# Optimization experiments

Measured on AMD Instinct MI355X. Metric: run time of the kernel, lower is better.

Reference implementation:

```python
import jax, jax.numpy as jnp
import numpy as np

NS, NT, E, B = 100000, 50000, 3200000, 16
F_E, F_XS, F_XT, F_U = 10, 10, 5, 10
H1 = F_E + F_XT            # 15, node_mlp_1 width
H2 = F_XS + 1 + 4 * H1 + F_U  # 81, node_mlp_2 input width


def leaky(x):
    return jnp.where(x > 0, x, 0.1 * x)


def setup_inputs() -> dict:
    key = jax.random.key(0)
    ks = jax.random.split(key, 16)
    s = 0.1
    return {
        "x_s": jax.random.normal(ks[0], (NS, F_XS), jnp.float32),
        "x_t": jax.random.normal(ks[1], (NT, F_XT), jnp.float32),
        "edge_attr": jax.random.normal(ks[2], (E, F_E), jnp.float32),
        "u": jax.random.normal(ks[3], (B, F_U), jnp.float32),
        "W1": jax.random.normal(ks[4], (H1, H1), jnp.float32) * s,
        "b1": jnp.zeros((H1,), jnp.float32),
        "W2": jax.random.normal(ks[5], (H1, H1), jnp.float32) * s,
        "b2": jnp.zeros((H1,), jnp.float32),
        "W3": jax.random.normal(ks[6], (H2, F_XS), jnp.float32) * s,
        "b3": jnp.zeros((F_XS,), jnp.float32),
        "W4": jax.random.normal(ks[7], (F_XS, F_XS), jnp.float32) * s,
        "b4": jnp.zeros((F_XS,), jnp.float32),
        "src_idx": jax.random.randint(ks[8], (E,), 0, NS, jnp.int32),
        "tgt_idx": jax.random.randint(ks[9], (E,), 0, NT, jnp.int32),
        "batch_s": jnp.sort(jax.random.randint(ks[10], (NS,), 0, B, jnp.int32)),
    }


def reference(x_s, x_t, edge_attr, u, W1, b1, W2, b2, W3, b3, W4, b4,
              src_idx, tgt_idx, batch_s):
    Ns = x_s.shape[0]
    # edge MLP: gather target features, concat edge attrs -> [E, 15]
    out = jnp.concatenate([x_t[tgt_idx], edge_attr], axis=1)
    out = leaky(out @ W1 + b1) @ W2 + b2

    # per-source-node counts; torch_scatter 'mean' divides by max(count, 1)
    n = jax.ops.segment_sum(jnp.ones((out.shape[0],), out.dtype), src_idx,
                            num_segments=Ns)
    denom = jnp.maximum(n, 1.0)[:, None]

    a = jax.ops.segment_sum(out, src_idx, num_segments=Ns) / denom           # mean
    m2 = jax.ops.segment_sum(out ** 2, src_idx, num_segments=Ns) / denom     # mean sq
    b = jnp.sqrt(1e-6 + jax.nn.relu(m2 - a ** 2))                            # std
    diff = out - a[src_idx]
    c = jax.ops.segment_sum(diff ** 3, src_idx, num_segments=Ns) / denom / b ** 3
    d = jax.ops.segment_sum(diff ** 4, src_idx, num_segments=Ns) / denom / b ** 4

    feat = jnp.concatenate([x_s, n[:, None], a, b, c, d, u[batch_s]], axis=1)  # [Ns, 81]
    return leaky(feat @ W3 + b3) @ W4 + b4
```

## Files before the change

### kernel.cpp

```cpp
#include <hip/hip_runtime.h>
#include <hip/hip_fp16.h>

#define H1 15
#define H2 81
#define FXS 10
#define FXT 5
#define FE 10
#define FU 10

#define BSH 7
#define NPB 128
#define MAXBUK 1024
#define ABLK 2048
#define TB1 1024
#define TBF 512
#define CAPS 5120

typedef _Float16 half4 __attribute__((ext_vector_type(4)));
typedef float floatx4 __attribute__((ext_vector_type(4)));
typedef unsigned int uint;
typedef unsigned short ushort;

__device__ __forceinline__ int sw(int row, int q) {
    return row * 8 + 2 * (q ^ ((row >> 2) & 3));
}

__global__ __launch_bounds__(256) void k_bhist(const int* __restrict__ src,
                                               int* __restrict__ bcnt, int E, int nbuk) {
    __shared__ int h[MAXBUK];
    for (int i = threadIdx.x; i < MAXBUK; i += 256) h[i] = 0;
    __syncthreads();
    for (int i = blockIdx.x * blockDim.x + threadIdx.x; i < E; i += gridDim.x * blockDim.x)
        atomicAdd(&h[src[i] >> BSH], 1);
    __syncthreads();
    for (int i = threadIdx.x; i < nbuk; i += 256)
        if (h[i]) atomicAdd(&bcnt[i], h[i]);
}

__global__ __launch_bounds__(1024) void k_bscan(const int* __restrict__ bcnt,
                                                int* __restrict__ boffs,
                                                int* __restrict__ bcur, int nbuk) {
    __shared__ int sc[MAXBUK];
    int t = threadIdx.x;
    int v = (t < nbuk) ? bcnt[t] : 0;
    sc[t] = v;
    __syncthreads();
    for (int d = 1; d < MAXBUK; d <<= 1) {
        int add = (t >= d) ? sc[t - d] : 0;
        __syncthreads();
        sc[t] += add;
        __syncthreads();
    }
    if (t < nbuk) { int o = sc[t] - v; boffs[t] = o; bcur[t] = o; }
}

__global__ __launch_bounds__(TB1, 8) void k_mlpbin(
    const float* __restrict__ x_t, const float* __restrict__ ea,
    const float* __restrict__ W1, const float* __restrict__ b1,
    const float* __restrict__ W2, const float* __restrict__ b2,
    const int* __restrict__ src, const int* __restrict__ tgt,
    int* __restrict__ bcur, uint* __restrict__ gbin, int E)
{
    __shared__ uint stagw[ABLK * 8];
    __shared__ int A[MAXBUK];
    __shared__ int B[MAXBUK];
    __shared__ ushort sbk[ABLK];
    __shared__ int wsum[16];

    int t = threadIdx.x;
    int lane = t & 63, w = t >> 6;
    int base = blockIdx.x * ABLK;
    int m = min(ABLK, E - base);

    int i0 = t, i1 = t + TB1;
    bool v0 = (i0 < m), v1 = (i1 < m);
    int e0 = base + (v0 ? i0 : 0);
    int e1 = base + (v1 ? i1 : 0);
    int sv0 = src[e0], tg0 = tgt[e0];
    int sv1 = src[e1], tg1 = tgt[e1];

    A[t] = 0;
    __syncthreads();
    if (v0) atomicAdd(&A[sv0 >> BSH], 1);
    if (v1) atomicAdd(&A[sv1 >> BSH], 1);

    float xt0[FXT], xt1[FXT];
    float2 ev0[5], ev1[5];
    {
        const float* xr0 = x_t + (size_t)tg0 * FXT;
        const float* xr1 = x_t + (size_t)tg1 * FXT;
#pragma unroll
        for (int j = 0; j < FXT; j++) { xt0[j] = xr0[j]; xt1[j] = xr1[j]; }
        const float2* er0 = (const float2*)(ea + (size_t)e0 * FE);
        const float2* er1 = (const float2*)(ea + (size_t)e1 * FE);
#pragma unroll
        for (int j = 0; j < 5; j++) { ev0[j] = er0[j]; ev1[j] = er1[j]; }
    }
    __syncthreads();

    int h = A[t];
    int x = h;
#pragma unroll
    for (int d = 1; d < 64; d <<= 1) {
        int y = __shfl_up(x, d, 64);
        if (lane >= d) x += y;
    }
    if (lane == 63) wsum[w] = x;
    __syncthreads();
    if (w == 0) {
        int v = (lane < 16) ? wsum[lane] : 0;
        int xx = v;
#pragma unroll
        for (int d = 1; d < 16; d <<= 1) {
            int y = __shfl_up(xx, d, 64);
            if (lane >= d) xx += y;
        }
        if (lane < 16) wsum[lane] = xx - v;
    }
    __syncthreads();
    int st = wsum[w] + (x - h);
    B[t] = st;
    int gb = h ? atomicAdd(&bcur[t], h) : 0;
    A[t] = gb - st;
    __syncthreads();

    int em = lane & 15;
    int kb = (lane >> 4) << 2;
    int q = kb >> 2;
    half4 a1f, a2f;
    floatx4 c1f, c2f;
#pragma unroll
    for (int i = 0; i < 4; i++) {
        int kk = kb + i;
        bool wv = (kk < H1) && (em < H1);
        a1f[i] = wv ? (_Float16)W1[kk * H1 + em] : (_Float16)0.f;
        a2f[i] = wv ? (_Float16)W2[kk * H1 + em] : (_Float16)0.f;
        c1f[i] = (kk < H1) ? b1[kk] : 0.f;
        c2f[i] = (kk < H1) ? b2[kk] : 0.f;
    }

#define STAGE_EDGE(sv, xt, ev)                                                  \
    {                                                                           \
        int bk = (sv) >> BSH;                                                   \
        int pos = atomicAdd(&B[bk], 1);                                         \
        sbk[pos] = (ushort)bk;                                                  \
        float f[15];                                                            \
        _Pragma("unroll")                                                       \
        for (int j = 0; j < FXT; j++) f[j] = (xt)[j];                           \
        _Pragma("unroll")                                                       \
        for (int j = 0; j < 5; j++) {                                           \
            f[FXT + 2 * j] = (ev)[j].x;                                         \
            f[FXT + 2 * j + 1] = (ev)[j].y;                                     \
        }                                                                       \
        _Pragma("unroll")                                                       \
        for (int c = 0; c < 4; c++) {                                           \
            union { _Float16 hh[4]; ushort us[4]; uint2 u; } pk;                \
            _Pragma("unroll")                                                   \
            for (int j = 0; j < 4; j++) {                                       \
                int fi = c * 4 + j;                                             \
                pk.hh[j] = (fi < 15) ? (_Float16)f[fi] : (_Float16)0.f;         \
            }                                                                   \
            if (c == 3) pk.us[3] = (ushort)((sv) & (NPB - 1));                  \
            *(uint2*)&stagw[sw(pos, c)] = pk.u;                                 \
        }                                                                       \
    }
    if (v0) STAGE_EDGE(sv0, xt0, ev0)
    if (v1) STAGE_EDGE(sv1, xt1, ev1)
#undef STAGE_EDGE
    __syncthreads();

#pragma unroll
    for (int g = 0; g < ABLK / (16 * 16); g++) {
        int r = w * 128 + g * 16 + em;
        union { uint2 u; _Float16 hh[4]; } bin_;
        bin_.u = *(uint2*)&stagw[sw(r, q)];
        half4 bf;
#pragma unroll
        for (int j = 0; j < 4; j++) bf[j] = bin_.hh[j];
        floatx4 d1 = __builtin_amdgcn_mfma_f32_16x16x16f16(a1f, bf, c1f, 0, 0, 0);
        half4 hm;
#pragma unroll
        for (int j = 0; j < 4; j++) {
            float xx = d1[j];
            xx = fmaxf(xx, 0.1f * xx);
            hm[j] = (_Float16)xx;
        }
        floatx4 d2 = __builtin_amdgcn_mfma_f32_16x16x16f16(a2f, hm, c2f, 0, 0, 0);
        union { _Float16 hh[4]; ushort us[4]; uint uu[2]; uint2 u; } ov;
#pragma unroll
        for (int j = 0; j < 4; j++) ov.hh[j] = (_Float16)d2[j];
        uint* wp = &stagw[sw(r, q)];
        if (kb < 12) {
            *(uint2*)wp = ov.u;
        } else {
            wp[0] = ov.uu[0];
            ((ushort*)&wp[1])[0] = ov.us[2];
        }
    }
    __syncthreads();

    for (int i = t; i < m; i += TB1) {
        int bk = sbk[i];
        uint2 q0 = *(uint2*)&stagw[sw(i, 0)];
        uint2 q1 = *(uint2*)&stagw[sw(i, 1)];
        uint2 q2 = *(uint2*)&stagw[sw(i, 2)];
        uint2 q3 = *(uint2*)&stagw[sw(i, 3)];
        size_t dst = (size_t)(A[bk] + i) * 8;
        *(uint4*)(gbin + dst)     = make_uint4(q0.x, q0.y, q1.x, q1.y);
        *(uint4*)(gbin + dst + 4) = make_uint4(q2.x, q2.y, q3.x, q3.y);
    }
}

__global__ __launch_bounds__(TBF, 6) void k_fuse(
    const float* __restrict__ x_s, const float* __restrict__ u,
    const float* __restrict__ W3, const float* __restrict__ b3,
    const float* __restrict__ W4, const float* __restrict__ b4,
    const int* __restrict__ batch_s,
    const int* __restrict__ bcnt, const int* __restrict__ boffs,
    const uint* __restrict__ gbin,
    float* __restrict__ out, int NSs)
{
    __shared__ ushort idx[CAPS];
    __shared__ int fh[NPB], fstart[NPB], fcur[NPB];
    __shared__ float sW3[H2 * FXS], sb3[FXS], sW4[FXS * FXS], sb4[FXS];
    __shared__ float feat[NPB][61];
    __shared__ float l1s[NPB][FXS];

    int t = threadIdx.x;
    for (int i = t; i < H2 * FXS; i += TBF) sW3[i] = W3[i];
    for (int i = t; i < FXS * FXS; i += TBF) sW4[i] = W4[i];
    if (t < FXS) { sb3[t] = b3[t]; sb4[t] = b4[t]; }
    if (t < NPB) fh[t] = 0;
    __syncthreads();

    int b = blockIdx.x;
    int base = boffs[b];
    int cnt = min(bcnt[b], CAPS);
    const uint* rb = gbin + (size_t)base * 8;

    for (int i = t; i < cnt; i += TBF)
        atomicAdd(&fh[(rb[(size_t)i * 8 + 7] >> 16) & (NPB - 1)], 1);
    __syncthreads();
    if (t < NPB) fstart[t] = fh[t];
    __syncthreads();
    for (int d = 1; d < NPB; d <<= 1) {
        int add = (t < NPB && t >= d) ? fstart[t - d] : 0;
        __syncthreads();
        if (t < NPB) fstart[t] += add;
        __syncthreads();
    }
    if (t < NPB) { int s0 = fstart[t] - fh[t]; fstart[t] = s0; fcur[t] = s0; }
    __syncthreads();
    for (int i = t; i < cnt; i += TBF) {
        int sl = (int)(rb[(size_t)i * 8 + 7] >> 16) & (NPB - 1);
        int p = atomicAdd(&fcur[sl], 1);
        idx[p] = (ushort)i;
    }
    __syncthreads();

    int l = t >> 2, lq = t & 3;
    int s = (b << BSH) + l;
    int n = fh[l], start = fstart[l];

    float s1[4] = {0.f,0.f,0.f,0.f}, s2[4] = {0.f,0.f,0.f,0.f};
    float s3[4] = {0.f,0.f,0.f,0.f}, s4[4] = {0.f,0.f,0.f,0.f};
    if (s < NSs) {
        for (int k = 0; k < n; k++) {
            int ri = idx[start + k];
            uint2 rv = *(const uint2*)(rb + (size_t)ri * 8 + lq * 2);
            union { uint uu[2]; _Float16 h[4]; } up;
            up.uu[0] = rv.x; up.uu[1] = rv.y;
#pragma unroll
            for (int j = 0; j < 4; j++) {
                float x = (float)up.h[j];
                float x2 = x * x;
                s1[j] += x;
                s2[j] = fmaf(x, x, s2[j]);
                s3[j] = fmaf(x2, x, s3[j]);
                s4[j] = fmaf(x2, x2, s4[j]);
            }
        }
        float inv = 1.0f / (float)(n > 1 ? n : 1);
#pragma unroll
        for (int j = 0; j < 4; j++) {
            int f = lq * 4 + j;
            if (f < H1) {
                float a = s1[j] * inv, m2 = s2[j] * inv, m3 = s3[j] * inv, m4 = s4[j] * inv;
                float a2 = a * a;
                float var = m2 - a2;
                float bb = sqrtf(1e-6f + fmaxf(var, 0.0f));
                float c3 = m3 - 3.0f * a * m2 + 2.0f * a * a2;
                float c4 = m4 - 4.0f * a * m3 + 6.0f * a2 * m2 - 3.0f * a2 * a2;
                float ib = 1.0f / bb, ib2 = ib * ib;
                feat[l][f * 4 + 0] = a;
                feat[l][f * 4 + 1] = bb;
                feat[l][f * 4 + 2] = c3 * ib * ib2;
                feat[l][f * 4 + 3] = c4 * ib2 * ib2;
            }
        }
        if (lq == 0) feat[l][60] = (float)n;
    }
    __syncthreads();

    for (int id = t; id < NPB * FXS; id += TBF) {
        int g = id / FXS, j = id - g * FXS;
        int ss = (b << BSH) + g;
        if (ss >= NSs) continue;
        const float* ar = feat[g];
        float acc = sb3[j];
        const float* xr = x_s + (size_t)ss * FXS;
#pragma unroll
        for (int i = 0; i < FXS; i++) acc = fmaf(xr[i], sW3[i * FXS + j], acc);
        acc = fmaf(ar[60], sW3[FXS * FXS + j], acc);
#pragma unroll
        for (int f = 0; f < H1; f++) {
            acc = fmaf(ar[f * 4 + 0], sW3[(11 + f) * FXS + j], acc);
            acc = fmaf(ar[f * 4 + 1], sW3[(26 + f) * FXS + j], acc);
            acc = fmaf(ar[f * 4 + 2], sW3[(41 + f) * FXS + j], acc);
            acc = fmaf(ar[f * 4 + 3], sW3[(56 + f) * FXS + j], acc);
        }
        const float* ur = u + (size_t)batch_s[ss] * FU;
#pragma unroll
        for (int i = 0; i < FU; i++) acc = fmaf(ur[i], sW3[(71 + i) * FXS + j], acc);
        l1s[g][j] = fmaxf(acc, 0.1f * acc);
    }
    __syncthreads();

    for (int id = t; id < NPB * FXS; id += TBF) {
        int g = id / FXS, j = id - g * FXS;
        int ss = (b << BSH) + g;
        if (ss >= NSs) continue;
        float acc = sb4[j];
#pragma unroll
        for (int i = 0; i < FXS; i++) acc = fmaf(l1s[g][i], sW4[i * FXS + j], acc);
        out[(size_t)ss * FXS + j] = acc;
    }
}

extern "C" void kernel_launch(void* const* d_in, const int* in_sizes, int n_in,
                              void* d_out, int out_size, void* d_ws, size_t ws_size,
                              hipStream_t stream) {
    const float* x_s = (const float*)d_in[0];
    const float* x_t = (const float*)d_in[1];
    const float* ea  = (const float*)d_in[2];
    const float* u   = (const float*)d_in[3];
    const float* W1  = (const float*)d_in[4];
    const float* b1  = (const float*)d_in[5];
    const float* W2  = (const float*)d_in[6];
    const float* b2  = (const float*)d_in[7];
    const float* W3  = (const float*)d_in[8];
    const float* b3  = (const float*)d_in[9];
    const float* W4  = (const float*)d_in[10];
    const float* b4  = (const float*)d_in[11];
    const int* src   = (const int*)d_in[12];
    const int* tgt   = (const int*)d_in[13];
    const int* batch_s = (const int*)d_in[14];

    int NSs = in_sizes[0] / FXS;
    int E   = in_sizes[2] / FE;
    int nbuk = (NSs + NPB - 1) >> BSH;

    auto align_up = [](size_t x) { return (x + 255) & ~(size_t)255; };
    char* w = (char*)d_ws;
    int* bcnt   = (int*)w; w += align_up((size_t)MAXBUK * 4);
    int* boffs  = (int*)w; w += align_up((size_t)MAXBUK * 4);
    int* bcur   = (int*)w; w += align_up((size_t)MAXBUK * 4);
    uint* gbin  = (uint*)w;

    hipMemsetAsync(bcnt, 0, (size_t)MAXBUK * 4, stream);

    k_bhist<<<512, 256, 0, stream>>>(src, bcnt, E, nbuk);
    k_bscan<<<1, 1024, 0, stream>>>(bcnt, boffs, bcur, nbuk);
    k_mlpbin<<<(E + ABLK - 1) / ABLK, TB1, 0, stream>>>(
        x_t, ea, W1, b1, W2, b2, src, tgt, bcur, gbin, E);
    k_fuse<<<nbuk, TBF, 0, stream>>>(
        x_s, u, W3, b3, W4, b4, batch_s, bcnt, boffs, gbin, (float*)d_out, NSs);
}
```

Before: 188.1 us.

## Double source-node bucket size to 256 and cache slot ids in fuse

```diff
diff --git a/kernel.cpp b/kernel.cpp
--- a/kernel.cpp
+++ b/kernel.cpp
@@ -8,13 +8,14 @@
 #define FE 10
 #define FU 10
 
-#define BSH 7
-#define NPB 128
-#define MAXBUK 1024
+#define BSH 8
+#define NPB 256
+#define MAXBUK 512
 #define ABLK 2048
 #define TB1 1024
 #define TBF 512
-#define CAPS 5120
+#define CAPS 10240
+#define RPT 20
 
 typedef _Float16 half4 __attribute__((ext_vector_type(4)));
 typedef float floatx4 __attribute__((ext_vector_type(4)));
@@ -37,9 +38,9 @@
         if (h[i]) atomicAdd(&bcnt[i], h[i]);
 }
 
-__global__ __launch_bounds__(1024) void k_bscan(const int* __restrict__ bcnt,
-                                                int* __restrict__ boffs,
-                                                int* __restrict__ bcur, int nbuk) {
+__global__ __launch_bounds__(MAXBUK) void k_bscan(const int* __restrict__ bcnt,
+                                                  int* __restrict__ boffs,
+                                                  int* __restrict__ bcur, int nbuk) {
     __shared__ int sc[MAXBUK];
     int t = threadIdx.x;
     int v = (t < nbuk) ? bcnt[t] : 0;
@@ -65,7 +66,7 @@
     __shared__ int A[MAXBUK];
     __shared__ int B[MAXBUK];
     __shared__ ushort sbk[ABLK];
-    __shared__ int wsum[16];
+    __shared__ int wsum[8];
 
     int t = threadIdx.x;
     int lane = t & 63, w = t >> 6;
@@ -79,7 +80,7 @@
     int sv0 = src[e0], tg0 = tgt[e0];
     int sv1 = src[e1], tg1 = tgt[e1];
 
-    A[t] = 0;
+    if (t < MAXBUK) A[t] = 0;
     __syncthreads();
     if (v0) atomicAdd(&A[sv0 >> BSH], 1);
     if (v1) atomicAdd(&A[sv1 >> BSH], 1);
@@ -98,30 +99,32 @@
     }
     __syncthreads();
 
-    int h = A[t];
-    int x = h;
+    int h = 0, x = 0;
+    if (t < MAXBUK) { h = A[t]; x = h; }
 #pragma unroll
     for (int d = 1; d < 64; d <<= 1) {
         int y = __shfl_up(x, d, 64);
         if (lane >= d) x += y;
     }
-    if (lane == 63) wsum[w] = x;
+    if (t < MAXBUK && lane == 63) wsum[w] = x;
     __syncthreads();
     if (w == 0) {
-        int v = (lane < 16) ? wsum[lane] : 0;
+        int v = (lane < 8) ? wsum[lane] : 0;
         int xx = v;
 #pragma unroll
-        for (int d = 1; d < 16; d <<= 1) {
+        for (int d = 1; d < 8; d <<= 1) {
             int y = __shfl_up(xx, d, 64);
             if (lane >= d) xx += y;
         }
-        if (lane < 16) wsum[lane] = xx - v;
-    }
-    __syncthreads();
-    int st = wsum[w] + (x - h);
-    B[t] = st;
-    int gb = h ? atomicAdd(&bcur[t], h) : 0;
-    A[t] = gb - st;
+        if (lane < 8) wsum[lane] = xx - v;
+    }
+    __syncthreads();
+    if (t < MAXBUK) {
+        int st = wsum[w] + (x - h);
+        B[t] = st;
+        int gb = h ? atomicAdd(&bcur[t], h) : 0;
+        A[t] = gb - st;
+    }
     __syncthreads();
 
     int em = lane & 15;
@@ -211,7 +214,7 @@
     }
 }
 
-__global__ __launch_bounds__(TBF, 6) void k_fuse(
+__global__ __launch_bounds__(TBF, 4) void k_fuse(
     const float* __restrict__ x_s, const float* __restrict__ u,
     const float* __restrict__ W3, const float* __restrict__ b3,
     const float* __restrict__ W4, const float* __restrict__ b4,
@@ -223,8 +226,8 @@
     __shared__ ushort idx[CAPS];
     __shared__ int fh[NPB], fstart[NPB], fcur[NPB];
     __shared__ float sW3[H2 * FXS], sb3[FXS], sW4[FXS * FXS], sb4[FXS];
-    __shared__ float feat[NPB][61];
-    __shared__ float l1s[NPB][FXS];
+    __shared__ float feat[128][61];
+    __shared__ float l1s[128][FXS];
 
     int t = threadIdx.x;
     for (int i = t; i < H2 * FXS; i += TBF) sW3[i] = W3[i];
@@ -238,8 +241,16 @@
     int cnt = min(bcnt[b], CAPS);
     const uint* rb = gbin + (size_t)base * 8;
 
-    for (int i = t; i < cnt; i += TBF)
-        atomicAdd(&fh[(rb[(size_t)i * 8 + 7] >> 16) & (NPB - 1)], 1);
+    int sid[RPT];
+#pragma unroll
+    for (int c = 0; c < RPT; c++) {
+        int i = t + c * TBF;
+        sid[c] = -1;
+        if (i < cnt) {
+            sid[c] = (int)(rb[(size_t)i * 8 + 7] >> 16) & (NPB - 1);
+            atomicAdd(&fh[sid[c]], 1);
+        }
+    }
     __syncthreads();
     if (t < NPB) fstart[t] = fh[t];
     __syncthreads();
@@ -251,89 +262,95 @@
     }
     if (t < NPB) { int s0 = fstart[t] - fh[t]; fstart[t] = s0; fcur[t] = s0; }
     __syncthreads();
-    for (int i = t; i < cnt; i += TBF) {
-        int sl = (int)(rb[(size_t)i * 8 + 7] >> 16) & (NPB - 1);
-        int p = atomicAdd(&fcur[sl], 1);
-        idx[p] = (ushort)i;
-    }
-    __syncthreads();
-
-    int l = t >> 2, lq = t & 3;
-    int s = (b << BSH) + l;
-    int n = fh[l], start = fstart[l];
-
-    float s1[4] = {0.f,0.f,0.f,0.f}, s2[4] = {0.f,0.f,0.f,0.f};
-    float s3[4] = {0.f,0.f,0.f,0.f}, s4[4] = {0.f,0.f,0.f,0.f};
-    if (s < NSs) {
-        for (int k = 0; k < n; k++) {
-            int ri = idx[start + k];
-            uint2 rv = *(const uint2*)(rb + (size_t)ri * 8 + lq * 2);
-            union { uint uu[2]; _Float16 h[4]; } up;
-            up.uu[0] = rv.x; up.uu[1] = rv.y;
+#pragma unroll
+    for (int c = 0; c < RPT; c++) {
+        if (sid[c] >= 0) {
+            int p = atomicAdd(&fcur[sid[c]], 1);
+            idx[p] = (ushort)(t + c * TBF);
+        }
+    }
+    __syncthreads();
+
+    for (int pass = 0; pass < 2; pass++) {
+        int l = t >> 2, lq = t & 3;
+        int ln = pass * 128 + l;
+        int s = (b << BSH) + ln;
+        int n = fh[ln], start = fstart[ln];
+
+        float s1[4] = {0.f,0.f,0.f,0.f}, s2[4] = {0.f,0.f,0.f,0.f};
+        float s3[4] = {0.f,0.f,0.f,0.f}, s4[4] = {0.f,0.f,0.f,0.f};
+        if (s < NSs) {
+            for (int k = 0; k < n; k++) {
+                int ri = idx[start + k];
+                uint2 rv = *(const uint2*)(rb + (size_t)ri * 8 + lq * 2);
+                union { uint uu[2]; _Float16 h[4]; } up;
+                up.uu[0] = rv.x; up.uu[1] = rv.y;
+#pragma unroll
+                for (int j = 0; j < 4; j++) {
+                    float x = (float)up.h[j];
+                    float x2 = x * x;
+                    s1[j] += x;
+                    s2[j] = fmaf(x, x, s2[j]);
+                    s3[j] = fmaf(x2, x, s3[j]);
+                    s4[j] = fmaf(x2, x2, s4[j]);
+                }
+            }
+            float inv = 1.0f / (float)(n > 1 ? n : 1);
 #pragma unroll
             for (int j = 0; j < 4; j++) {
-                float x = (float)up.h[j];
-                float x2 = x * x;
-                s1[j] += x;
-                s2[j] = fmaf(x, x, s2[j]);
-                s3[j] = fmaf(x2, x, s3[j]);
-                s4[j] = fmaf(x2, x2, s4[j]);
+                int f = lq * 4 + j;
+                if (f < H1) {
+                    float a = s1[j] * inv, m2 = s2[j] * inv, m3 = s3[j] * inv, m4 = s4[j] * inv;
+                    float a2 = a * a;
+                    float var = m2 - a2;
+                    float bb = sqrtf(1e-6f + fmaxf(var, 0.0f));
+                    float c3 = m3 - 3.0f * a * m2 + 2.0f * a * a2;
+                    float c4 = m4 - 4.0f * a * m3 + 6.0f * a2 * m2 - 3.0f * a2 * a2;
+                    float ib = 1.0f / bb, ib2 = ib * ib;
+                    feat[l][f * 4 + 0] = a;
+                    feat[l][f * 4 + 1] = bb;
+                    feat[l][f * 4 + 2] = c3 * ib * ib2;
+                    feat[l][f * 4 + 3] = c4 * ib2 * ib2;
+                }
             }
-        }
-        float inv = 1.0f / (float)(n > 1 ? n : 1);
-#pragma unroll
-        for (int j = 0; j < 4; j++) {
-            int f = lq * 4 + j;
-            if (f < H1) {
-                float a = s1[j] * inv, m2 = s2[j] * inv, m3 = s3[j] * inv, m4 = s4[j] * inv;
-                float a2 = a * a;
-                float var = m2 - a2;
-                float bb = sqrtf(1e-6f + fmaxf(var, 0.0f));
-                float c3 = m3 - 3.0f * a * m2 + 2.0f * a * a2;
-                float c4 = m4 - 4.0f * a * m3 + 6.0f * a2 * m2 - 3.0f * a2 * a2;
-                float ib = 1.0f / bb, ib2 = ib * ib;
-                feat[l][f * 4 + 0] = a;
-                feat[l][f * 4 + 1] = bb;
-                feat[l][f * 4 + 2] = c3 * ib * ib2;
-                feat[l][f * 4 + 3] = c4 * ib2 * ib2;
+            if (lq == 0) feat[l][60] = (float)n;
+        }
+        __syncthreads();
+
+        for (int id = t; id < 128 * FXS; id += TBF) {
+            int g = id / FXS, j = id - g * FXS;
+            int ss = (b << BSH) + pass * 128 + g;
+            if (ss >= NSs) continue;
+            const float* ar = feat[g];
+            float acc = sb3[j];
+            const float* xr = x_s + (size_t)ss * FXS;
+#pragma unroll
+            for (int i = 0; i < FXS; i++) acc = fmaf(xr[i], sW3[i * FXS + j], acc);
+            acc = fmaf(ar[60], sW3[FXS * FXS + j], acc);
+#pragma unroll
+            for (int f = 0; f < H1; f++) {
+                acc = fmaf(ar[f * 4 + 0], sW3[(11 + f) * FXS + j], acc);
+                acc = fmaf(ar[f * 4 + 1], sW3[(26 + f) * FXS + j], acc);
+                acc = fmaf(ar[f * 4 + 2], sW3[(41 + f) * FXS + j], acc);
+                acc = fmaf(ar[f * 4 + 3], sW3[(56 + f) * FXS + j], acc);
             }
-        }
-        if (lq == 0) feat[l][60] = (float)n;
-    }
-    __syncthreads();
-
-    for (int id = t; id < NPB * FXS; id += TBF) {
-        int g = id / FXS, j = id - g * FXS;
-        int ss = (b << BSH) + g;
-        if (ss >= NSs) continue;
-        const float* ar = feat[g];
-        float acc = sb3[j];
-        const float* xr = x_s + (size_t)ss * FXS;
-#pragma unroll
-        for (int i = 0; i < FXS; i++) acc = fmaf(xr[i], sW3[i * FXS + j], acc);
-        acc = fmaf(ar[60], sW3[FXS * FXS + j], acc);
-#pragma unroll
-        for (int f = 0; f < H1; f++) {
-            acc = fmaf(ar[f * 4 + 0], sW3[(11 + f) * FXS + j], acc);
-            acc = fmaf(ar[f * 4 + 1], sW3[(26 + f) * FXS + j], acc);
-            acc = fmaf(ar[f * 4 + 2], sW3[(41 + f) * FXS + j], acc);
-            acc = fmaf(ar[f * 4 + 3], sW3[(56 + f) * FXS + j], acc);
-        }
-        const float* ur = u + (size_t)batch_s[ss] * FU;
-#pragma unroll
-        for (int i = 0; i < FU; i++) acc = fmaf(ur[i], sW3[(71 + i) * FXS + j], acc);
-        l1s[g][j] = fmaxf(acc, 0.1f * acc);
-    }
-    __syncthreads();
-
-    for (int id = t; id < NPB * FXS; id += TBF) {
-        int g = id / FXS, j = id - g * FXS;
-        int ss = (b << BSH) + g;
-        if (ss >= NSs) continue;
-        float acc = sb4[j];
-#pragma unroll
-        for (int i = 0; i < FXS; i++) acc = fmaf(l1s[g][i], sW4[i * FXS + j], acc);
-        out[(size_t)ss * FXS + j] = acc;
+            const float* ur = u + (size_t)batch_s[ss] * FU;
+#pragma unroll
+            for (int i = 0; i < FU; i++) acc = fmaf(ur[i], sW3[(71 + i) * FXS + j], acc);
+            l1s[g][j] = fmaxf(acc, 0.1f * acc);
+        }
+        __syncthreads();
+
+        for (int id = t; id < 128 * FXS; id += TBF) {
+            int g = id / FXS, j = id - g * FXS;
+            int ss = (b << BSH) + pass * 128 + g;
+            if (ss >= NSs) continue;
+            float acc = sb4[j];
+#pragma unroll
+            for (int i = 0; i < FXS; i++) acc = fmaf(l1s[g][i], sW4[i * FXS + j], acc);
+            out[(size_t)ss * FXS + j] = acc;
+        }
+        __syncthreads();
     }
 }
 
@@ -370,7 +387,7 @@
     hipMemsetAsync(bcnt, 0, (size_t)MAXBUK * 4, stream);
 
     k_bhist<<<512, 256, 0, stream>>>(src, bcnt, E, nbuk);
-    k_bscan<<<1, 1024, 0, stream>>>(bcnt, boffs, bcur, nbuk);
+    k_bscan<<<1, MAXBUK, 0, stream>>>(bcnt, boffs, bcur, nbuk);
     k_mlpbin<<<(E + ABLK - 1) / ABLK, TB1, 0, stream>>>(
         x_t, ea, W1, b1, W2, b2, src, tgt, bcur, gbin, E);
     k_fuse<<<nbuk, TBF, 0, stream>>>(
```

Result: faster. 172.5 us (median of 2 runs) (-8.3%).
